# Kernel tuning notes

Measured on AMD Instinct MI355X. Metric: run time of the kernel, lower is better.

The kernel has to match this reference:

```python
import jax, jax.numpy as jnp
import numpy as np

N = 100000  # num nodes


def _gcn_conv(x, src, dst, W, b, n_nodes):
    """PyG GCNConv: symmetric normalization with implicit self-loops.
    out = D^{-1/2} (A + I) D^{-1/2} (x W) + b, deg counts in-edges + self-loop.
    """
    h = x @ W  # [N, H]
    ones = jnp.ones(src.shape[0], dtype=x.dtype)
    deg = jax.ops.segment_sum(ones, dst, num_segments=n_nodes) + 1.0  # +1 self-loop
    dinv = jax.lax.rsqrt(deg)  # [N]
    norm = dinv[src] * dinv[dst]  # [E]
    msg = h[src] * norm[:, None]  # gather + scale: memory-bound
    agg = jax.ops.segment_sum(msg, dst, num_segments=n_nodes)
    agg = agg + h * (dinv * dinv)[:, None]  # self-loop contribution
    return agg + b


def setup_inputs() -> dict:
    key = jax.random.key(0)
    k1, k2, k3, k4 = jax.random.split(key, 4)
    F = 64
    E = 1600000
    x = jax.random.normal(k1, (N, F), dtype=jnp.float32)
    edge_index = jax.random.randint(k2, (2, E), 0, N, dtype=jnp.int64)
    W1 = jax.random.normal(k3, (F, F), dtype=jnp.float32) / jnp.sqrt(jnp.float32(F))
    b1 = jnp.zeros((F,), dtype=jnp.float32)
    W2 = jax.random.normal(k4, (F, F), dtype=jnp.float32) / jnp.sqrt(jnp.float32(F))
    b2 = jnp.zeros((F,), dtype=jnp.float32)
    return {"x": x, "edge_index": edge_index, "W1": W1, "b1": b1, "W2": W2, "b2": b2}


def reference(x, edge_index, W1, b1, W2, b2):
    src, dst = edge_index[0], edge_index[1]
    h = _gcn_conv(x, src, dst, W1, b1, N)
    h = jax.nn.relu(h)
    # dropout(p=0.1) is identity in eval mode
    h = _gcn_conv(h, src, dst, W2, b2, N)
    return jax.nn.relu(h)
```

## Files before the change

### kernel.cpp

```cpp
#include <hip/hip_runtime.h>
#include <hip/hip_bf16.h>
#include <stdint.h>

#define NN 100000
#define NE 1600000
#define NBLK 256
#define EPB (NE / NBLK)
#define NBINS 782
#define NCELL (NBINS * NBLK)
#define NSB ((NCELL + 1023) / 1024)
#define GEMMB 782
#define BINCAP 4096


__device__ __forceinline__ unsigned pack_bf16(float a, float b) {
    unsigned ua = __float_as_uint(a);
    unsigned ub = __float_as_uint(b);
    ua += 0x7FFFu + ((ua >> 16) & 1u);
    ub += 0x7FFFu + ((ub >> 16) & 1u);
    return (ua >> 16) | (ub & 0xFFFF0000u);
}
#define BF_LO(u) __uint_as_float((u) << 16)
#define BF_HI(u) __uint_as_float((u) & 0xFFFF0000u)


__device__ __forceinline__ int ei_is64(const int* __restrict__ ei) {
    int z = 0;
#pragma unroll
    for (int i = 0; i < 16; ++i) z |= ei[2 * i + 1];
    return z == 0;
}


__global__ void __launch_bounds__(1024) k_hist(const int* __restrict__ ei,
                                               int* __restrict__ gcount) {
    __shared__ int lbin[NBINS];
    int t = threadIdx.x, blk = blockIdx.x;
    for (int i = t; i < NBINS; i += 1024) lbin[i] = 0;
    __syncthreads();
    int is64 = ei_is64(ei);
    int e0 = blk * EPB;
    if (is64) {
        const int2* p = (const int2*)ei;
        for (int e = e0 + t; e < e0 + EPB; e += 1024)
            atomicAdd(&lbin[p[NE + e].x >> 7], 1);
    } else {
        for (int e = e0 + t; e < e0 + EPB; e += 1024)
            atomicAdd(&lbin[ei[NE + e] >> 7], 1);
    }
    __syncthreads();
    for (int b = t; b < NBINS; b += 1024) gcount[b * NBLK + blk] = lbin[b];
}

__global__ void k_pscan1(const int* __restrict__ g, int* __restrict__ bsum) {
    __shared__ int sh[256];
    int t = threadIdx.x;
    int base = blockIdx.x * 1024 + t * 4;
    int s = 0;
#pragma unroll
    for (int j = 0; j < 4; ++j) { int i = base + j; if (i < NCELL) s += g[i]; }
    sh[t] = s; __syncthreads();
    for (int off = 128; off > 0; off >>= 1) {
        if (t < off) sh[t] += sh[t + off];
        __syncthreads();
    }
    if (t == 0) bsum[blockIdx.x] = sh[0];
}

__global__ void k_pscan23(const int* __restrict__ g, const int* __restrict__ bsum,
                          int* __restrict__ goff) {
    __shared__ int sh[256];
    __shared__ int boffs;
    int t = threadIdx.x;
    int bv = (t < NSB) ? bsum[t] : 0;
    sh[t] = bv; __syncthreads();
    for (int off = 1; off < 256; off <<= 1) {
        int tmp = (t >= off) ? sh[t - off] : 0;
        __syncthreads();
        sh[t] += tmp;
        __syncthreads();
    }
    if (t == blockIdx.x) boffs = sh[t] - bv;
    __syncthreads();
    int base = blockIdx.x * 1024 + t * 4;
    int v[4]; int s = 0;
#pragma unroll
    for (int j = 0; j < 4; ++j) { int i = base + j; v[j] = (i < NCELL) ? g[i] : 0; s += v[j]; }
    __syncthreads();
    sh[t] = s; __syncthreads();
    for (int off = 1; off < 256; off <<= 1) {
        int tmp = (t >= off) ? sh[t - off] : 0;
        __syncthreads();
        sh[t] += tmp;
        __syncthreads();
    }
    int run = sh[t] - s + boffs;
#pragma unroll
    for (int j = 0; j < 4; ++j) {
        int i = base + j;
        if (i < NCELL) { goff[i] = run; run += v[j]; }
    }
}

__global__ void __launch_bounds__(1024) k_scatter(const int* __restrict__ ei,
                                                  const int* __restrict__ goff,
                                                  unsigned* __restrict__ tmp) {
    __shared__ int gpos[NBINS];
    int t = threadIdx.x, blk = blockIdx.x;
    for (int i = t; i < NBINS; i += 1024) gpos[i] = goff[i * NBLK + blk];
    __syncthreads();
    int is64 = ei_is64(ei);
    int e0 = blk * EPB;
    for (int e = e0 + t; e < e0 + EPB; e += 1024) {
        int s, d;
        if (is64) {
            s = ((const int2*)ei)[e].x;
            d = ((const int2*)ei)[NE + e].x;
        } else {
            s = ei[e];
            d = ei[NE + e];
        }
        int b = d >> 7;
        int pos = atomicAdd(&gpos[b], 1);
        tmp[pos] = (unsigned)s | ((unsigned)(d & 127) << 17);
    }
}


__device__ __forceinline__ void gemm_body(int gb, const float* __restrict__ X,
                                          const float* __restrict__ W,
                                          unsigned* __restrict__ Hb) {
    int wid = (gb * 256 + (int)threadIdx.x) >> 6;
    int lane = threadIdx.x & 63;
    int task = __builtin_amdgcn_readfirstlane(wid);
    const int ntasks = ((NN + 63) >> 6) * 2;
    if (task >= ntasks) return;
    int t = task >> 1;
    int ch = task & 1;
    int row = t * 64 + lane;
    int r = row < NN ? row : NN - 1;
    const float4* xp = (const float4*)(X + (size_t)r * 64);
    const float* Wb = W + ch * 32;
    float acc[32];
#pragma unroll
    for (int c = 0; c < 32; ++c) acc[c] = 0.f;
#pragma unroll 4
    for (int k4 = 0; k4 < 16; ++k4) {
        float4 xv = xp[k4];
#pragma unroll
        for (int kj = 0; kj < 4; ++kj) {
            float xk = (kj == 0) ? xv.x : (kj == 1) ? xv.y : (kj == 2) ? xv.z : xv.w;
            const float4* wr = (const float4*)(Wb + (k4 * 4 + kj) * 64);
#pragma unroll
            for (int c4 = 0; c4 < 8; ++c4) {
                float4 wv = wr[c4];
                acc[c4 * 4 + 0] += xk * wv.x;
                acc[c4 * 4 + 1] += xk * wv.y;
                acc[c4 * 4 + 2] += xk * wv.z;
                acc[c4 * 4 + 3] += xk * wv.w;
            }
        }
    }
    uint4* op = (uint4*)(Hb + (size_t)r * 32 + ch * 16);
#pragma unroll
    for (int q = 0; q < 4; ++q) {
        uint4 o;
        o.x = pack_bf16(acc[q * 8 + 0], acc[q * 8 + 1]);
        o.y = pack_bf16(acc[q * 8 + 2], acc[q * 8 + 3]);
        o.z = pack_bf16(acc[q * 8 + 4], acc[q * 8 + 5]);
        o.w = pack_bf16(acc[q * 8 + 6], acc[q * 8 + 7]);
        op[q] = o;
    }
}

__global__ void __launch_bounds__(256) k_gemm(const float* __restrict__ X,
                                              const float* __restrict__ W,
                                              unsigned* __restrict__ Hb) {
    gemm_body(blockIdx.x, X, W, Hb);
}


__global__ void __launch_bounds__(256) k_degcsr_gemm(const unsigned* __restrict__ tmp,
                                                     const int* __restrict__ goff,
                                                     int* __restrict__ rs,
                                                     float* __restrict__ dinv,
                                                     unsigned* __restrict__ csr,
                                                     const float* __restrict__ X,
                                                     const float* __restrict__ W1,
                                                     unsigned* __restrict__ Hb) {
    if (blockIdx.x >= NBINS) {
        gemm_body((int)blockIdx.x - NBINS, X, W1, Hb);
        return;
    }
    __shared__ unsigned cache[BINCAP];
    __shared__ int hist[128];
    __shared__ int cur[128];
    __shared__ int base_sh[128];
    int b = blockIdx.x, t = threadIdx.x;
    if (t < 128) { hist[t] = 0; cur[t] = 0; }
    __syncthreads();
    int bs = goff[b * NBLK];
    int be = (b == NBINS - 1) ? NE : goff[(b + 1) * NBLK];
    for (int e = bs + t; e < be; e += 256) {
        unsigned v = tmp[e];
        int i = e - bs;
        if (i < BINCAP) cache[i] = v;
        atomicAdd(&hist[v >> 17], 1);
    }
    __syncthreads();
    if (t < 128) {
        int node = b * 128 + t;
        if (node < NN) {
            int c = hist[t];
            int loff = 0;
            for (int i = 0; i < t; ++i) loff += hist[i];
            rs[node] = bs + loff;
            base_sh[t] = bs + loff;
            dinv[node] = rsqrtf((float)c + 1.0f);
        } else base_sh[t] = 0;
    }
    if (b == 0 && t == 0) rs[NN] = NE;
    __syncthreads();
    int cnt = be - bs;
    for (int i = t; i < cnt; i += 256) {
        unsigned v = (i < BINCAP) ? cache[i] : tmp[bs + i];
        int dl = v >> 17;
        int lr = atomicAdd(&cur[dl], 1);
        csr[base_sh[dl] + lr] = v & 0x1FFFFu;
    }
}


#define EDGE_ACC(wt, r)                                                       \
    {                                                                         \
        a0 += BF_LO((r).x) * (wt); a1 += BF_HI((r).x) * (wt);                 \
        a2 += BF_LO((r).y) * (wt); a3 += BF_HI((r).y) * (wt);                 \
        a4 += BF_LO((r).z) * (wt); a5 += BF_HI((r).z) * (wt);                 \
        a6 += BF_LO((r).w) * (wt); a7 += BF_HI((r).w) * (wt);                 \
    }

__global__ void __launch_bounds__(256) k_agg(const uint4* __restrict__ hb,
                                             const int* __restrict__ rs,
                                             const unsigned* __restrict__ csr,
                                             const float* __restrict__ dinv,
                                             const float* __restrict__ bias,
                                             float4* __restrict__ out4) {
    int wid = (blockIdx.x * blockDim.x + threadIdx.x) >> 6;
    int lane = threadIdx.x & 63;
    int node = __builtin_amdgcn_readfirstlane(wid);
    if (node >= NN) return;
    int g = lane >> 3;
    int s = lane & 7;
    const char* hbc = (const char*)hb;
    const char* dvc = (const char*)dinv;
    unsigned soff = (unsigned)s << 4;
    float dn = dinv[node];
    int e0 = rs[node], e1 = rs[node + 1];
    float a0 = 0.f, a1 = 0.f, a2 = 0.f, a3 = 0.f;
    float a4 = 0.f, a5 = 0.f, a6 = 0.f, a7 = 0.f;
    int e = e0 + g;
    unsigned p0 = csr[e];
    unsigned p1 = csr[e + 8];
    for (; e + 8 < e1; e += 16) {
        unsigned q0 = csr[e + 16];
        unsigned q1 = csr[e + 24];
        float w0 = *(const float*)(dvc + (size_t)(p0 << 2));
        float w1 = *(const float*)(dvc + (size_t)(p1 << 2));
        uint4 r0 = *(const uint4*)(hbc + (size_t)((p0 << 7) + soff));
        uint4 r1 = *(const uint4*)(hbc + (size_t)((p1 << 7) + soff));
        EDGE_ACC(w0, r0);
        EDGE_ACC(w1, r1);
        p0 = q0; p1 = q1;
    }
    if (e < e1) {
        float w0 = *(const float*)(dvc + (size_t)(p0 << 2));
        uint4 r0 = *(const uint4*)(hbc + (size_t)((p0 << 7) + soff));
        EDGE_ACC(w0, r0);
    }
#pragma unroll
    for (int m = 8; m <= 32; m <<= 1) {
        a0 += __shfl_xor(a0, m); a1 += __shfl_xor(a1, m);
        a2 += __shfl_xor(a2, m); a3 += __shfl_xor(a3, m);
        a4 += __shfl_xor(a4, m); a5 += __shfl_xor(a5, m);
        a6 += __shfl_xor(a6, m); a7 += __shfl_xor(a7, m);
    }
    if (lane < 8) {
        uint4 r = hb[(size_t)node * 8 + s];
        const float4* bp = (const float4*)(bias + s * 8);
        float4 b0 = bp[0], b1v = bp[1];
        float4 o0, o1;
        o0.x = fmaxf((a0 + BF_LO(r.x) * dn) * dn + b0.x, 0.f);
        o0.y = fmaxf((a1 + BF_HI(r.x) * dn) * dn + b0.y, 0.f);
        o0.z = fmaxf((a2 + BF_LO(r.y) * dn) * dn + b0.z, 0.f);
        o0.w = fmaxf((a3 + BF_HI(r.y) * dn) * dn + b0.w, 0.f);
        o1.x = fmaxf((a4 + BF_LO(r.z) * dn) * dn + b1v.x, 0.f);
        o1.y = fmaxf((a5 + BF_HI(r.z) * dn) * dn + b1v.y, 0.f);
        o1.z = fmaxf((a6 + BF_LO(r.w) * dn) * dn + b1v.z, 0.f);
        o1.w = fmaxf((a7 + BF_HI(r.w) * dn) * dn + b1v.w, 0.f);
        out4[(size_t)node * 16 + s * 2] = o0;
        out4[(size_t)node * 16 + s * 2 + 1] = o1;
    }
}


extern "C" void kernel_launch(void* const* d_in, const int* in_sizes, int n_in,
                              void* d_out, int out_size, void* d_ws, size_t ws_size,
                              hipStream_t stream) {
    const float* x  = (const float*)d_in[0];
    const int* ei   = (const int*)d_in[1];
    const float* W1 = (const float*)d_in[2];
    const float* b1 = (const float*)d_in[3];
    const float* W2 = (const float*)d_in[4];
    const float* b2 = (const float*)d_in[5];

    char* ws = (char*)d_ws;
    size_t off = 0;
    auto alloc = [&](size_t bytes) -> char* {
        char* p = ws + off;
        off = (off + bytes + 511) & ~(size_t)511;
        return p;
    };
    int*      gcount= (int*)alloc((size_t)NCELL * 4);
    int*      goff  = (int*)alloc((size_t)NCELL * 4);
    int*      bsum  = (int*)alloc((size_t)NSB * 4);
    unsigned* tmp   = (unsigned*)alloc((size_t)NE * 4);
    unsigned* csr   = (unsigned*)alloc((size_t)NE * 4);
    int*      rs    = (int*)alloc((size_t)(NN + 1) * 4);
    float*    dinv  = (float*)alloc((size_t)NN * 4);
    unsigned* hbuf  = (unsigned*)alloc((size_t)NN * 32 * 4);
    float*    hmid  = (float*)d_out;

    k_hist<<<NBLK, 1024, 0, stream>>>(ei, gcount);
    k_pscan1<<<NSB, 256, 0, stream>>>(gcount, bsum);
    k_pscan23<<<NSB, 256, 0, stream>>>(gcount, bsum, goff);
    k_scatter<<<NBLK, 1024, 0, stream>>>(ei, goff, tmp);
    k_degcsr_gemm<<<NBINS + GEMMB, 256, 0, stream>>>(tmp, goff, rs, dinv, csr,
                                                     x, W1, hbuf);
    k_agg<<<(NN * 64) / 256, 256, 0, stream>>>((const uint4*)hbuf, rs, csr, dinv, b1,
                                               (float4*)hmid);
    k_gemm<<<GEMMB, 256, 0, stream>>>(hmid, W2, hbuf);
    k_agg<<<(NN * 64) / 256, 256, 0, stream>>>((const uint4*)hbuf, rs, csr, dinv, b2,
                                               (float4*)d_out);
}
```

Measured before the change: 240.1 us.

## Fuse layer-2 GEMM into layer-1 aggregation epilogue via wave shuffles

The first aggregation kernel now computes the bias+ReLU output per node and immediately multiplies it by W2 inside the same wavefront, using shuffles to broadcast the 64 features and each lane computing one output column. It writes bf16 H2 directly to a new buffer. This removes the fp32 intermediate write/read and a separate GEMM launch. In exchange it adds 64 shuffles and 64 W2 loads per wave (cached), and extra work in the epilogue of a memory-bound kernel.

```diff
diff --git a/kernel.cpp b/kernel.cpp
--- a/kernel.cpp
+++ b/kernel.cpp
@@ -173,12 +173,6 @@
     }
 }
 
-__global__ void __launch_bounds__(256) k_gemm(const float* __restrict__ X,
-                                              const float* __restrict__ W,
-                                              unsigned* __restrict__ Hb) {
-    gemm_body(blockIdx.x, X, W, Hb);
-}
-
 
 __global__ void __launch_bounds__(256) k_degcsr_gemm(const unsigned* __restrict__ tmp,
                                                      const int* __restrict__ goff,
@@ -239,53 +233,56 @@
         a6 += BF_LO((r).w) * (wt); a7 += BF_HI((r).w) * (wt);                 \
     }
 
-__global__ void __launch_bounds__(256) k_agg(const uint4* __restrict__ hb,
+#define AGG_BODY(hb_, rs_, csr_, dinv_)                                       \
+    int wid = (blockIdx.x * blockDim.x + threadIdx.x) >> 6;                   \
+    int lane = threadIdx.x & 63;                                              \
+    int node = __builtin_amdgcn_readfirstlane(wid);                           \
+    if (node >= NN) return;                                                   \
+    int g = lane >> 3;                                                        \
+    int s = lane & 7;                                                         \
+    const char* hbc = (const char*)(hb_);                                     \
+    const char* dvc = (const char*)(dinv_);                                   \
+    unsigned soff = (unsigned)s << 4;                                         \
+    float dn = (dinv_)[node];                                                 \
+    int e0 = (rs_)[node], e1 = (rs_)[node + 1];                               \
+    float a0 = 0.f, a1 = 0.f, a2 = 0.f, a3 = 0.f;                             \
+    float a4 = 0.f, a5 = 0.f, a6 = 0.f, a7 = 0.f;                             \
+    int e = e0 + g;                                                           \
+    unsigned p0 = (csr_)[e];                                                  \
+    unsigned p1 = (csr_)[e + 8];                                              \
+    for (; e + 8 < e1; e += 16) {                                             \
+        unsigned q0 = (csr_)[e + 16];                                         \
+        unsigned q1 = (csr_)[e + 24];                                         \
+        float w0 = *(const float*)(dvc + (size_t)(p0 << 2));                  \
+        float w1 = *(const float*)(dvc + (size_t)(p1 << 2));                  \
+        uint4 r0 = *(const uint4*)(hbc + (size_t)((p0 << 7) + soff));         \
+        uint4 r1 = *(const uint4*)(hbc + (size_t)((p1 << 7) + soff));         \
+        EDGE_ACC(w0, r0);                                                     \
+        EDGE_ACC(w1, r1);                                                     \
+        p0 = q0; p1 = q1;                                                     \
+    }                                                                         \
+    if (e < e1) {                                                             \
+        float w0 = *(const float*)(dvc + (size_t)(p0 << 2));                  \
+        uint4 r0 = *(const uint4*)(hbc + (size_t)((p0 << 7) + soff));         \
+        EDGE_ACC(w0, r0);                                                     \
+    }                                                                         \
+    _Pragma("unroll")                                                         \
+    for (int m = 8; m <= 32; m <<= 1) {                                       \
+        a0 += __shfl_xor(a0, m); a1 += __shfl_xor(a1, m);                     \
+        a2 += __shfl_xor(a2, m); a3 += __shfl_xor(a3, m);                     \
+        a4 += __shfl_xor(a4, m); a5 += __shfl_xor(a5, m);                     \
+        a6 += __shfl_xor(a6, m); a7 += __shfl_xor(a7, m);                     \
+    }
+
+__global__ void __launch_bounds__(256) k_agg(const unsigned* __restrict__ hb,
                                              const int* __restrict__ rs,
                                              const unsigned* __restrict__ csr,
                                              const float* __restrict__ dinv,
                                              const float* __restrict__ bias,
                                              float4* __restrict__ out4) {
-    int wid = (blockIdx.x * blockDim.x + threadIdx.x) >> 6;
-    int lane = threadIdx.x & 63;
-    int node = __builtin_amdgcn_readfirstlane(wid);
-    if (node >= NN) return;
-    int g = lane >> 3;
-    int s = lane & 7;
-    const char* hbc = (const char*)hb;
-    const char* dvc = (const char*)dinv;
-    unsigned soff = (unsigned)s << 4;
-    float dn = dinv[node];
-    int e0 = rs[node], e1 = rs[node + 1];
-    float a0 = 0.f, a1 = 0.f, a2 = 0.f, a3 = 0.f;
-    float a4 = 0.f, a5 = 0.f, a6 = 0.f, a7 = 0.f;
-    int e = e0 + g;
-    unsigned p0 = csr[e];
-    unsigned p1 = csr[e + 8];
-    for (; e + 8 < e1; e += 16) {
-        unsigned q0 = csr[e + 16];
-        unsigned q1 = csr[e + 24];
-        float w0 = *(const float*)(dvc + (size_t)(p0 << 2));
-        float w1 = *(const float*)(dvc + (size_t)(p1 << 2));
-        uint4 r0 = *(const uint4*)(hbc + (size_t)((p0 << 7) + soff));
-        uint4 r1 = *(const uint4*)(hbc + (size_t)((p1 << 7) + soff));
-        EDGE_ACC(w0, r0);
-        EDGE_ACC(w1, r1);
-        p0 = q0; p1 = q1;
-    }
-    if (e < e1) {
-        float w0 = *(const float*)(dvc + (size_t)(p0 << 2));
-        uint4 r0 = *(const uint4*)(hbc + (size_t)((p0 << 7) + soff));
-        EDGE_ACC(w0, r0);
-    }
-#pragma unroll
-    for (int m = 8; m <= 32; m <<= 1) {
-        a0 += __shfl_xor(a0, m); a1 += __shfl_xor(a1, m);
-        a2 += __shfl_xor(a2, m); a3 += __shfl_xor(a3, m);
-        a4 += __shfl_xor(a4, m); a5 += __shfl_xor(a5, m);
-        a6 += __shfl_xor(a6, m); a7 += __shfl_xor(a7, m);
-    }
+    AGG_BODY(hb, rs, csr, dinv)
     if (lane < 8) {
-        uint4 r = hb[(size_t)node * 8 + s];
+        uint4 r = *(const uint4*)(hbc + (size_t)(((unsigned)node << 7) + soff));
         const float4* bp = (const float4*)(bias + s * 8);
         float4 b0 = bp[0], b1v = bp[1];
         float4 o0, o1;
@@ -300,6 +297,38 @@
         out4[(size_t)node * 16 + s * 2] = o0;
         out4[(size_t)node * 16 + s * 2 + 1] = o1;
     }
+}
+
+__global__ void __launch_bounds__(256) k_agg_gemm(const unsigned* __restrict__ hb,
+                                                  const int* __restrict__ rs,
+                                                  const unsigned* __restrict__ csr,
+                                                  const float* __restrict__ dinv,
+                                                  const float* __restrict__ bias,
+                                                  const float* __restrict__ W2,
+                                                  unsigned* __restrict__ Hb2) {
+    AGG_BODY(hb, rs, csr, dinv)
+    uint4 r = *(const uint4*)(hbc + (size_t)(((unsigned)node << 7) + soff));
+    const float4* bp = (const float4*)(bias + s * 8);
+    float4 b0 = bp[0], b1v = bp[1];
+    float o[8];
+    o[0] = fmaxf((a0 + BF_LO(r.x) * dn) * dn + b0.x, 0.f);
+    o[1] = fmaxf((a1 + BF_HI(r.x) * dn) * dn + b0.y, 0.f);
+    o[2] = fmaxf((a2 + BF_LO(r.y) * dn) * dn + b0.z, 0.f);
+    o[3] = fmaxf((a3 + BF_HI(r.y) * dn) * dn + b0.w, 0.f);
+    o[4] = fmaxf((a4 + BF_LO(r.z) * dn) * dn + b1v.x, 0.f);
+    o[5] = fmaxf((a5 + BF_HI(r.z) * dn) * dn + b1v.y, 0.f);
+    o[6] = fmaxf((a6 + BF_LO(r.w) * dn) * dn + b1v.z, 0.f);
+    o[7] = fmaxf((a7 + BF_HI(r.w) * dn) * dn + b1v.w, 0.f);
+    const float* w2 = W2 + lane;
+    float gacc = 0.f;
+#pragma unroll
+    for (int k = 0; k < 64; ++k) {
+        float rk = __shfl(o[k & 7], k >> 3);
+        gacc += rk * w2[k * 64];
+    }
+    float gn = __shfl_xor(gacc, 1);
+    if (!(lane & 1))
+        Hb2[(size_t)node * 32 + (lane >> 1)] = pack_bf16(gacc, gn);
 }
 
 
@@ -328,7 +357,7 @@
     int*      rs    = (int*)alloc((size_t)(NN + 1) * 4);
     float*    dinv  = (float*)alloc((size_t)NN * 4);
     unsigned* hbuf  = (unsigned*)alloc((size_t)NN * 32 * 4);
-    float*    hmid  = (float*)d_out;
+    unsigned* hbuf2 = (unsigned*)alloc((size_t)NN * 32 * 4);
 
     k_hist<<<NBLK, 1024, 0, stream>>>(ei, gcount);
     k_pscan1<<<NSB, 256, 0, stream>>>(gcount, bsum);
@@ -336,9 +365,8 @@
     k_scatter<<<NBLK, 1024, 0, stream>>>(ei, goff, tmp);
     k_degcsr_gemm<<<NBINS + GEMMB, 256, 0, stream>>>(tmp, goff, rs, dinv, csr,
                                                      x, W1, hbuf);
-    k_agg<<<(NN * 64) / 256, 256, 0, stream>>>((const uint4*)hbuf, rs, csr, dinv, b1,
-                                               (float4*)hmid);
-    k_gemm<<<GEMMB, 256, 0, stream>>>(hmid, W2, hbuf);
-    k_agg<<<(NN * 64) / 256, 256, 0, stream>>>((const uint4*)hbuf, rs, csr, dinv, b2,
+    k_agg_gemm<<<(NN * 64) / 256, 256, 0, stream>>>(hbuf, rs, csr, dinv, b1, W2,
+                                                    hbuf2);
+    k_agg<<<(NN * 64) / 256, 256, 0, stream>>>(hbuf2, rs, csr, dinv, b2,
                                                (float4*)d_out);
 }
```

New measurement: 270.7 us. 1.13x slower.

## Fuse histogram, prefix scan and scatter into one persistent kernel with grid barriers

Applied to the files above, without the earlier changes.

Merges the four CSR-build kernels (histogram, two scan passes, scatter) into a single 256-block kernel that uses atomic-counter grid barriers between phases. The goal is to remove three kernel launch gaps and the tail idle time between them. In exchange it needs a memset of the barrier counters and depends on all 256 blocks of 1024 threads being resident at once, or it deadlocks. The self-loop load in k_agg also changes to byte-offset addressing.

```diff
diff --git a/kernel.cpp b/kernel.cpp
--- a/kernel.cpp
+++ b/kernel.cpp
@@ -32,14 +32,32 @@
 }
 
 
-__global__ void __launch_bounds__(1024) k_hist(const int* __restrict__ ei,
-                                               int* __restrict__ gcount) {
+__device__ __forceinline__ void gbar(int* bar, int id) {
+    __syncthreads();
+    if (threadIdx.x == 0) {
+        __threadfence();
+        __hip_atomic_fetch_add(&bar[id], 1, __ATOMIC_ACQ_REL, __HIP_MEMORY_SCOPE_AGENT);
+        while (__hip_atomic_load(&bar[id], __ATOMIC_ACQUIRE, __HIP_MEMORY_SCOPE_AGENT) < NBLK) {}
+        __threadfence();
+    }
+    __syncthreads();
+}
+
+
+__global__ void __launch_bounds__(1024) k_build(const int* __restrict__ ei,
+                                                int* __restrict__ gcount,
+                                                int* __restrict__ bsum,
+                                                int* __restrict__ goff,
+                                                unsigned* __restrict__ tmp,
+                                                int* __restrict__ bar) {
     __shared__ int lbin[NBINS];
+    __shared__ int sh[256];
+    __shared__ int boffs_sh;
     int t = threadIdx.x, blk = blockIdx.x;
-    for (int i = t; i < NBINS; i += 1024) lbin[i] = 0;
-    __syncthreads();
     int is64 = ei_is64(ei);
     int e0 = blk * EPB;
+    for (int i = t; i < NBINS; i += 1024) lbin[i] = 0;
+    __syncthreads();
     if (is64) {
         const int2* p = (const int2*)ei;
         for (int e = e0 + t; e < e0 + EPB; e += 1024)
@@ -50,67 +68,64 @@
     }
     __syncthreads();
     for (int b = t; b < NBINS; b += 1024) gcount[b * NBLK + blk] = lbin[b];
-}
-
-__global__ void k_pscan1(const int* __restrict__ g, int* __restrict__ bsum) {
-    __shared__ int sh[256];
-    int t = threadIdx.x;
-    int base = blockIdx.x * 1024 + t * 4;
-    int s = 0;
-#pragma unroll
-    for (int j = 0; j < 4; ++j) { int i = base + j; if (i < NCELL) s += g[i]; }
-    sh[t] = s; __syncthreads();
-    for (int off = 128; off > 0; off >>= 1) {
-        if (t < off) sh[t] += sh[t + off];
-        __syncthreads();
-    }
-    if (t == 0) bsum[blockIdx.x] = sh[0];
-}
-
-__global__ void k_pscan23(const int* __restrict__ g, const int* __restrict__ bsum,
-                          int* __restrict__ goff) {
-    __shared__ int sh[256];
-    __shared__ int boffs;
-    int t = threadIdx.x;
-    int bv = (t < NSB) ? bsum[t] : 0;
-    sh[t] = bv; __syncthreads();
-    for (int off = 1; off < 256; off <<= 1) {
-        int tmp = (t >= off) ? sh[t - off] : 0;
-        __syncthreads();
-        sh[t] += tmp;
-        __syncthreads();
-    }
-    if (t == blockIdx.x) boffs = sh[t] - bv;
-    __syncthreads();
-    int base = blockIdx.x * 1024 + t * 4;
-    int v[4]; int s = 0;
-#pragma unroll
-    for (int j = 0; j < 4; ++j) { int i = base + j; v[j] = (i < NCELL) ? g[i] : 0; s += v[j]; }
-    __syncthreads();
-    sh[t] = s; __syncthreads();
-    for (int off = 1; off < 256; off <<= 1) {
-        int tmp = (t >= off) ? sh[t - off] : 0;
-        __syncthreads();
-        sh[t] += tmp;
-        __syncthreads();
-    }
-    int run = sh[t] - s + boffs;
-#pragma unroll
-    for (int j = 0; j < 4; ++j) {
-        int i = base + j;
-        if (i < NCELL) { goff[i] = run; run += v[j]; }
-    }
-}
-
-__global__ void __launch_bounds__(1024) k_scatter(const int* __restrict__ ei,
-                                                  const int* __restrict__ goff,
-                                                  unsigned* __restrict__ tmp) {
-    __shared__ int gpos[NBINS];
-    int t = threadIdx.x, blk = blockIdx.x;
-    for (int i = t; i < NBINS; i += 1024) gpos[i] = goff[i * NBLK + blk];
-    __syncthreads();
-    int is64 = ei_is64(ei);
-    int e0 = blk * EPB;
+    gbar(bar, 0);
+    if (blk < NSB) {
+        if (t < 256) {
+            int base = blk * 1024 + t * 4;
+            int s = 0;
+#pragma unroll
+            for (int j = 0; j < 4; ++j) { int i = base + j; if (i < NCELL) s += gcount[i]; }
+            sh[t] = s;
+        }
+        __syncthreads();
+        for (int off = 128; off > 0; off >>= 1) {
+            if (t < off) sh[t] += sh[t + off];
+            __syncthreads();
+        }
+        if (t == 0) bsum[blk] = sh[0];
+    }
+    gbar(bar, 1);
+    if (blk < NSB) {
+        int bv = 0;
+        if (t < 256) { bv = (t < NSB) ? bsum[t] : 0; sh[t] = bv; }
+        __syncthreads();
+        for (int off = 1; off < 256; off <<= 1) {
+            int tv = 0;
+            if (t < 256 && t >= off) tv = sh[t - off];
+            __syncthreads();
+            if (t < 256) sh[t] += tv;
+            __syncthreads();
+        }
+        if (t == blk) boffs_sh = sh[t] - bv;
+        __syncthreads();
+        int v[4]; int s = 0;
+        int base = blk * 1024 + t * 4;
+        if (t < 256) {
+#pragma unroll
+            for (int j = 0; j < 4; ++j) { int i = base + j; v[j] = (i < NCELL) ? gcount[i] : 0; s += v[j]; }
+        }
+        __syncthreads();
+        if (t < 256) sh[t] = s;
+        __syncthreads();
+        for (int off = 1; off < 256; off <<= 1) {
+            int tv = 0;
+            if (t < 256 && t >= off) tv = sh[t - off];
+            __syncthreads();
+            if (t < 256) sh[t] += tv;
+            __syncthreads();
+        }
+        if (t < 256) {
+            int run = sh[t] - s + boffs_sh;
+#pragma unroll
+            for (int j = 0; j < 4; ++j) {
+                int i = base + j;
+                if (i < NCELL) { goff[i] = run; run += v[j]; }
+            }
+        }
+    }
+    gbar(bar, 2);
+    for (int i = t; i < NBINS; i += 1024) lbin[i] = goff[i * NBLK + blk];
+    __syncthreads();
     for (int e = e0 + t; e < e0 + EPB; e += 1024) {
         int s, d;
         if (is64) {
@@ -121,7 +136,7 @@
             d = ei[NE + e];
         }
         int b = d >> 7;
-        int pos = atomicAdd(&gpos[b], 1);
+        int pos = atomicAdd(&lbin[b], 1);
         tmp[pos] = (unsigned)s | ((unsigned)(d & 127) << 17);
     }
 }
@@ -239,7 +254,7 @@
         a6 += BF_LO((r).w) * (wt); a7 += BF_HI((r).w) * (wt);                 \
     }
 
-__global__ void __launch_bounds__(256) k_agg(const uint4* __restrict__ hb,
+__global__ void __launch_bounds__(256) k_agg(const unsigned* __restrict__ hb,
                                              const int* __restrict__ rs,
                                              const unsigned* __restrict__ csr,
                                              const float* __restrict__ dinv,
@@ -285,7 +300,7 @@
         a6 += __shfl_xor(a6, m); a7 += __shfl_xor(a7, m);
     }
     if (lane < 8) {
-        uint4 r = hb[(size_t)node * 8 + s];
+        uint4 r = *(const uint4*)(hbc + (size_t)(((unsigned)node << 7) + soff));
         const float4* bp = (const float4*)(bias + s * 8);
         float4 b0 = bp[0], b1v = bp[1];
         float4 o0, o1;
@@ -320,6 +335,7 @@
         off = (off + bytes + 511) & ~(size_t)511;
         return p;
     };
+    int*      bar   = (int*)alloc(64);
     int*      gcount= (int*)alloc((size_t)NCELL * 4);
     int*      goff  = (int*)alloc((size_t)NCELL * 4);
     int*      bsum  = (int*)alloc((size_t)NSB * 4);
@@ -330,15 +346,13 @@
     unsigned* hbuf  = (unsigned*)alloc((size_t)NN * 32 * 4);
     float*    hmid  = (float*)d_out;
 
-    k_hist<<<NBLK, 1024, 0, stream>>>(ei, gcount);
-    k_pscan1<<<NSB, 256, 0, stream>>>(gcount, bsum);
-    k_pscan23<<<NSB, 256, 0, stream>>>(gcount, bsum, goff);
-    k_scatter<<<NBLK, 1024, 0, stream>>>(ei, goff, tmp);
+    hipMemsetAsync(bar, 0, 64, stream);
+    k_build<<<NBLK, 1024, 0, stream>>>(ei, gcount, bsum, goff, tmp, bar);
     k_degcsr_gemm<<<NBINS + GEMMB, 256, 0, stream>>>(tmp, goff, rs, dinv, csr,
                                                      x, W1, hbuf);
-    k_agg<<<(NN * 64) / 256, 256, 0, stream>>>((const uint4*)hbuf, rs, csr, dinv, b1,
+    k_agg<<<(NN * 64) / 256, 256, 0, stream>>>(hbuf, rs, csr, dinv, b1,
                                                (float4*)hmid);
     k_gemm<<<GEMMB, 256, 0, stream>>>(hmid, W2, hbuf);
-    k_agg<<<(NN * 64) / 256, 256, 0, stream>>>((const uint4*)hbuf, rs, csr, dinv, b2,
+    k_agg<<<(NN * 64) / 256, 256, 0, stream>>>(hbuf, rs, csr, dinv, b2,
                                                (float4*)d_out);
 }
```

Measured after the change: 331.2 us. 37.9% more time.
